# Optimization experiments

Measured on AMD Instinct MI355X. Metric: run time of the kernel, lower is better.

Reference implementation:

```python
import jax, jax.numpy as jnp
import numpy as np

B, S, D = 4, 4096, 1024
H = 8                    # num_heads
DK = D // H              # head_k_dim = 128
DV = D // H              # head_v_dim = 128
KLEPE = 5                # lepe kernel size
ROPE_BASE = 10000.0


def rotate_half(x):
    x1, x2 = jnp.split(x, 2, axis=-1)
    return jnp.concatenate([-x2, x1], axis=-1)


def rope_sin_cos(seq_len, dim):
    inv_freq = 1.0 / (ROPE_BASE ** (jnp.arange(0, dim, 2, dtype=jnp.float32) / dim))
    freqs = jnp.arange(seq_len, dtype=jnp.float32)[:, None] * inv_freq[None, :]
    emb = jnp.concatenate([freqs, freqs], axis=-1)  # [S, dim]
    return jnp.sin(emb), jnp.cos(emb)


def mala_attn(q, k, v):
    """Magnitude-aware linear attention with inline RoPE.

    Attention weights A_ij = (scale*q_i.k_j + 1) / (scale*q_i.(sum_j k_j) + S):
    rows sum to 1 but, unlike plain linear attention, the sharpness of the
    distribution still depends on ||q_i|| (magnitude rectification). Computed
    in O(S*d^2) linear form without materializing the SxS matrix.
    q, k: [B,S,H,DK]; v: [B,S,H,DV].
    """
    sin, cos = rope_sin_cos(q.shape[1], q.shape[-1])
    sin, cos = sin[None, :, None, :], cos[None, :, None, :]
    q = q * cos + rotate_half(q) * sin
    k = k * cos + rotate_half(k) * sin
    scale = q.shape[-1] ** -0.5
    seq_len = q.shape[1]
    kv = jnp.einsum('bshd,bshe->bhde', k, v)      # [B,H,DK,DV]
    ksum = k.sum(axis=1)                          # [B,H,DK]
    vsum = v.sum(axis=1)                          # [B,H,DV]
    num = jnp.einsum('bshd,bhde->bshe', q, kv) * scale + vsum[:, None, :, :]
    den = jnp.einsum('bshd,bhd->bsh', q, ksum) * scale + seq_len
    return num / den[..., None]


def lepe_conv(v, w, b):
    # depthwise Conv1d over the sequence axis; channel id = h*DV + d
    Bb, Ss = v.shape[0], v.shape[1]
    x = v.transpose(0, 2, 3, 1).reshape(Bb, H * DV, Ss)   # [B, C, S]
    y = jax.lax.conv_general_dilated(
        x, w, window_strides=(1,), padding=[(KLEPE // 2, KLEPE // 2)],
        dimension_numbers=('NCH', 'OIH', 'NCH'), feature_group_count=H * DV)
    y = y + b[None, :, None]
    return y.reshape(Bb, H, DV, Ss).transpose(0, 3, 1, 2)  # [B,S,H,DV]


def setup_inputs() -> dict:
    key = jax.random.key(0)
    ks = jax.random.split(key, 8)
    w = 0.02
    return {
        'hidden_states': jax.random.normal(ks[0], (B, S, D), dtype=jnp.float32),
        'Wq': jax.random.normal(ks[1], (D, D), dtype=jnp.float32) * w,
        'Wk': jax.random.normal(ks[2], (D, D), dtype=jnp.float32) * w,
        'Wv': jax.random.normal(ks[3], (D, D), dtype=jnp.float32) * w,
        'Wg': jax.random.normal(ks[4], (D, D), dtype=jnp.float32) * w,
        'Wo': jax.random.normal(ks[5], (D, D), dtype=jnp.float32) * w,
        'lepe_w': jax.random.normal(ks[6], (D, 1, KLEPE), dtype=jnp.float32) * 0.1,
        'lepe_b': jnp.zeros((D,), dtype=jnp.float32),
    }


def reference(hidden_states, Wq, Wk, Wv, Wg, Wo, lepe_w, lepe_b):
    Bb, Ss, _ = hidden_states.shape
    q = (hidden_states @ Wq.T).reshape(Bb, Ss, H, DK)
    k = (hidden_states @ Wk.T).reshape(Bb, Ss, H, DK)
    v = (hidden_states @ Wv.T).reshape(Bb, Ss, H, DV)
    o_gate = hidden_states @ Wg.T                          # [B,S,D]
    o = mala_attn(q, k, v) + lepe_conv(v, lepe_w, lepe_b)  # [B,S,H,DV]
    o = o.reshape(Bb, Ss, H * DV) * o_gate
    return o @ Wo.T
```

## Files before the change

kernel.cpp:

```cpp
#include <hip/hip_runtime.h>
#include <math.h>
#include <stdint.h>


typedef __bf16 bf16;
typedef __bf16 bf16x2 __attribute__((ext_vector_type(2)));
typedef __bf16 bf16x4 __attribute__((ext_vector_type(4)));
typedef __bf16 bf16x8 __attribute__((ext_vector_type(8)));
typedef float f32x4 __attribute__((ext_vector_type(4)));

static constexpr float kScale = 0.08838834764831845f;

__device__ __forceinline__ void async_copy16(const void* g, void* l) {
  __builtin_amdgcn_global_load_lds(
      (const __attribute__((address_space(1))) void*)(uintptr_t)g,
      (__attribute__((address_space(3))) void*)(uintptr_t)l, 16, 0, 0);
}

__global__ __launch_bounds__(256, 2) void gemm_qkvg(
    const bf16* __restrict__ A, const bf16* __restrict__ Bw,
    bf16* __restrict__ C, const float2* __restrict__ tab)
{
  __shared__ __align__(16) char smem[17408];
  bf16* As = (bf16*)smem;
  bf16* Bs = (bf16*)(smem + 8192);
  bf16* T  = (bf16*)smem;

  const int t = threadIdx.x;
  const int bid = blockIdx.x;
  const int xcd = bid & 7, n = bid >> 3;
  const int bx = xcd * 16 + (n & 15);
  const int by = n >> 4;
  const long m0 = (long)bx * 128;
  A  += m0 * 1024;
  Bw += (long)by * 131072;
  C  += m0 * 4096 + (long)by * 128;

  const int i0 = t, i1 = t + 256;
  const bf16* gA0 = A  + (long)(i0 >> 2) * 1024 + (i0 & 3) * 8;
  const bf16* gA1 = A  + (long)(i1 >> 2) * 1024 + (i1 & 3) * 8;
  const bf16* gB0 = Bw + (long)(i0 >> 2) * 1024 + (i0 & 3) * 8;
  const bf16* gB1 = Bw + (long)(i1 >> 2) * 1024 + (i1 & 3) * 8;
  bf16* lA0 = As + i0 * 8; bf16* lA1 = As + i1 * 8;
  bf16* lB0 = Bs + i0 * 8; bf16* lB1 = Bs + i1 * 8;

  const int lane = t & 63, wv = t >> 6;
  const int moff = (wv & 1) * 64, noff = (wv >> 1) * 64;
  const int fm = lane & 15, fq = lane >> 4;

  f32x4 acc[4][4] = {};

  for (int k0 = 0; k0 < 1024; k0 += 32) {
    async_copy16(gA0, lA0); async_copy16(gA1, lA1);
    async_copy16(gB0, lB0); async_copy16(gB1, lB1);
    gA0 += 32; gA1 += 32; gB0 += 32; gB1 += 32;
    __syncthreads();
    bf16x8 af[4], bfv[4];
#pragma unroll
    for (int i = 0; i < 4; ++i) {
      af[i]  = *(const bf16x8*)(As + (moff + i * 16 + fm) * 32 + fq * 8);
      bfv[i] = *(const bf16x8*)(Bs + (noff + i * 16 + fm) * 32 + fq * 8);
    }
#pragma unroll
    for (int i = 0; i < 4; ++i)
#pragma unroll
      for (int j = 0; j < 4; ++j)
        acc[i][j] = __builtin_amdgcn_mfma_f32_16x16x32_bf16(af[i], bfv[j], acc[i][j], 0, 0, 0);
    __syncthreads();
  }

#pragma unroll
  for (int half = 0; half < 2; ++half) {
    if ((wv & 1) == half) {
#pragma unroll
      for (int i = 0; i < 4; ++i)
#pragma unroll
        for (int j = 0; j < 4; ++j)
#pragma unroll
          for (int r = 0; r < 4; ++r)
            T[(i * 16 + fq * 4 + r) * 136 + noff + j * 16 + fm] = (bf16)acc[i][j][r];
    }
    __syncthreads();
    if (by < 16) {
#pragma unroll
      for (int it = 0; it < 16; ++it) {
        const int pi = t + it * 256;
        const int row = pi >> 6, i = pi & 63;
        const int s = (int)((m0 + half * 64 + row) & 4095);
        const float2 sc = tab[s * 64 + i];
        float x1 = (float)T[row * 136 + i];
        float x2 = (float)T[row * 136 + i + 64];
        T[row * 136 + i]      = (bf16)(x1 * sc.y - x2 * sc.x);
        T[row * 136 + i + 64] = (bf16)(x2 * sc.y + x1 * sc.x);
      }
      __syncthreads();
    }
    const int srow0 = t >> 4, sc0 = (t & 15) * 8;
#pragma unroll
    for (int it = 0; it < 4; ++it) {
      const int row = it * 16 + srow0;
      *(bf16x8*)(C + (long)(half * 64 + row) * 4096 + sc0) = *(const bf16x8*)(T + row * 136 + sc0);
    }
    __syncthreads();
  }
}

__global__ __launch_bounds__(256, 2) void gemm_final(
    const bf16* __restrict__ A, const bf16* __restrict__ Bw,
    float* __restrict__ C)
{
  __shared__ __align__(16) bf16 As[128 * 32];
  __shared__ __align__(16) bf16 Bs[128 * 32];
  const int t = threadIdx.x;
  const int bid = blockIdx.x;
  const int xcd = bid & 7, n = bid >> 3;
  const int bx = xcd * 16 + (n & 15);
  const int by = n >> 4;
  const long m0 = (long)bx * 128;
  A  += m0 * 1024;
  Bw += (long)by * 131072;
  C  += m0 * 1024 + (long)by * 128;

  const int i0 = t, i1 = t + 256;
  const bf16* gA0 = A  + (long)(i0 >> 2) * 1024 + (i0 & 3) * 8;
  const bf16* gA1 = A  + (long)(i1 >> 2) * 1024 + (i1 & 3) * 8;
  const bf16* gB0 = Bw + (long)(i0 >> 2) * 1024 + (i0 & 3) * 8;
  const bf16* gB1 = Bw + (long)(i1 >> 2) * 1024 + (i1 & 3) * 8;
  bf16* lA0 = As + i0 * 8; bf16* lA1 = As + i1 * 8;
  bf16* lB0 = Bs + i0 * 8; bf16* lB1 = Bs + i1 * 8;

  const int lane = t & 63, wv = t >> 6;
  const int moff = (wv & 1) * 64, noff = (wv >> 1) * 64;
  const int fm = lane & 15, fq = lane >> 4;

  f32x4 acc[4][4] = {};

  for (int k0 = 0; k0 < 1024; k0 += 32) {
    async_copy16(gA0, lA0); async_copy16(gA1, lA1);
    async_copy16(gB0, lB0); async_copy16(gB1, lB1);
    gA0 += 32; gA1 += 32; gB0 += 32; gB1 += 32;
    __syncthreads();
    bf16x8 af[4], bfv[4];
#pragma unroll
    for (int i = 0; i < 4; ++i) {
      af[i]  = *(const bf16x8*)(As + (moff + i * 16 + fm) * 32 + fq * 8);
      bfv[i] = *(const bf16x8*)(Bs + (noff + i * 16 + fm) * 32 + fq * 8);
    }
#pragma unroll
    for (int i = 0; i < 4; ++i)
#pragma unroll
      for (int j = 0; j < 4; ++j)
        acc[i][j] = __builtin_amdgcn_mfma_f32_16x16x32_bf16(af[i], bfv[j], acc[i][j], 0, 0, 0);
    __syncthreads();
  }

#pragma unroll
  for (int i = 0; i < 4; ++i)
#pragma unroll
    for (int j = 0; j < 4; ++j)
#pragma unroll
      for (int r = 0; r < 4; ++r)
        C[(long)(moff + i * 16 + fq * 4 + r) * 1024 + noff + j * 16 + fm] = acc[i][j][r];
}

__global__ __launch_bounds__(256, 2) void gemm_num(
    const bf16* __restrict__ QKVG, const bf16* __restrict__ kvTall,
    const float* __restrict__ ksum, const float* __restrict__ vsum,
    const float* __restrict__ lepe_w, const float* __restrict__ lepe_b,
    bf16* __restrict__ obuf)
{
  __shared__ __align__(16) char smem[17408];
  bf16* As = (bf16*)smem;
  bf16* Bs = (bf16*)(smem + 8192);
  bf16* T  = (bf16*)smem;
  __shared__ float sden[128], svsum[128], slb[128], sksum[128];
  __shared__ float slw[5][128];

  const int t = threadIdx.x;
  const int h = blockIdx.y, b = blockIdx.z;
  const int bh = b * 8 + h;
  const long m0 = (long)blockIdx.x * 128;
  const bf16* A  = QKVG + (long)b * 16777216 + m0 * 4096 + h * 128;
  const bf16* Bw = kvTall + (long)bh * 16384;

  if (t < 128) {
    sksum[t] = ksum[bh * 128 + t];
    svsum[t] = vsum[bh * 128 + t];
    slb[t]   = lepe_b[h * 128 + t];
#pragma unroll
    for (int j = 0; j < 5; ++j) slw[j][t] = lepe_w[(h * 128 + t) * 5 + j];
  }

  const int i0 = t, i1 = t + 256;
  const bf16* gA0 = A + (long)(i0 >> 2) * 4096 + (i0 & 3) * 8;
  const bf16* gA1 = A + (long)(i1 >> 2) * 4096 + (i1 & 3) * 8;
  const bf16* gB0 = Bw + (long)(i0 >> 2) * 128 + (i0 & 3) * 8;
  const bf16* gB1 = Bw + (long)(i1 >> 2) * 128 + (i1 & 3) * 8;
  bf16* lA0 = As + i0 * 8; bf16* lA1 = As + i1 * 8;
  bf16* lB0 = Bs + i0 * 8; bf16* lB1 = Bs + i1 * 8;

  const int lane = t & 63, wv = t >> 6;
  const int moff = (wv & 1) * 64, noff = (wv >> 1) * 64;
  const int fm = lane & 15, fq = lane >> 4;

  f32x4 acc[4][4] = {};
  float dacc = 0.f;

  for (int k0 = 0; k0 < 128; k0 += 32) {
    async_copy16(gA0, lA0); async_copy16(gA1, lA1);
    async_copy16(gB0, lB0); async_copy16(gB1, lB1);
    gA0 += 32; gA1 += 32; gB0 += 32; gB1 += 32;
    __syncthreads();
    bf16x8 af[4], bfv[4];
#pragma unroll
    for (int i = 0; i < 4; ++i) {
      af[i]  = *(const bf16x8*)(As + (moff + i * 16 + fm) * 32 + fq * 8);
      bfv[i] = *(const bf16x8*)(Bs + (noff + i * 16 + fm) * 32 + fq * 8);
    }
#pragma unroll
    for (int i = 0; i < 4; ++i)
#pragma unroll
      for (int j = 0; j < 4; ++j)
        acc[i][j] = __builtin_amdgcn_mfma_f32_16x16x32_bf16(af[i], bfv[j], acc[i][j], 0, 0, 0);
    if (t < 128) {
#pragma unroll
      for (int c8 = 0; c8 < 4; ++c8) {
        bf16x8 q8 = *(const bf16x8*)(As + t * 32 + c8 * 8);
#pragma unroll
        for (int e = 0; e < 8; ++e) dacc += (float)q8[e] * sksum[k0 + c8 * 8 + e];
      }
    }
    __syncthreads();
  }
  if (t < 128) sden[t] = dacc * kScale + 4096.0f;

  const int c2 = lane * 2;
  const float w0[5] = {slw[0][c2], slw[1][c2], slw[2][c2], slw[3][c2], slw[4][c2]};
  const float w1[5] = {slw[0][c2+1], slw[1][c2+1], slw[2][c2+1], slw[3][c2+1], slw[4][c2+1]};
  const float lb0 = slb[c2], lb1 = slb[c2 + 1];

#pragma unroll
  for (int half = 0; half < 2; ++half) {
    if ((wv & 1) == half) {
#pragma unroll
      for (int i = 0; i < 4; ++i)
#pragma unroll
        for (int j = 0; j < 4; ++j)
#pragma unroll
          for (int r = 0; r < 4; ++r) {
            const int col = noff + j * 16 + fm;
            T[(i * 16 + fq * 4 + r) * 136 + col] = (bf16)(acc[i][j][r] * kScale + svsum[col]);
          }
    }
    __syncthreads();
    for (int rr = 0; rr < 16; ++rr) {
      const int lrow = wv * 16 + rr;
      const int row = half * 64 + lrow;
      const int s = (int)(m0 + row);
      const long grow = (long)b * 4096 + s;
      const float rden = 1.0f / sden[row];
      const bf16* vrow = QKVG + grow * 4096 + 2048 + h * 128 + c2;
      bf16x2 a2 = *(const bf16x2*)(T + lrow * 136 + c2);
      float lep0 = lb0, lep1 = lb1;
#pragma unroll
      for (int jt = 0; jt < 5; ++jt) {
        const int srow = s + jt - 2;
        if (srow >= 0 && srow < 4096) {
          bf16x2 v2 = *(const bf16x2*)(vrow + (long)(jt - 2) * 4096);
          lep0 += (float)v2[0] * w0[jt];
          lep1 += (float)v2[1] * w1[jt];
        }
      }
      bf16x2 g2 = *(const bf16x2*)(QKVG + grow * 4096 + 3072 + h * 128 + c2);
      bf16x2 o2;
      o2[0] = (bf16)(((float)a2[0] * rden + lep0) * (float)g2[0]);
      o2[1] = (bf16)(((float)a2[1] * rden + lep1) * (float)g2[1]);
      *(bf16x2*)(obuf + grow * 1024 + h * 128 + c2) = o2;
    }
    __syncthreads();
  }
}

__global__ void prep_kernel(const float* __restrict__ X, const float* __restrict__ Wq,
                            const float* __restrict__ Wk, const float* __restrict__ Wv,
                            const float* __restrict__ Wg, const float* __restrict__ Wo,
                            bf16* __restrict__ Xb, bf16* __restrict__ Wcat,
                            bf16* __restrict__ Wob, float2* __restrict__ tab)
{
  const int blk = blockIdx.x;
  if (blk < 16384) {
    long g = ((long)blk * 256 + threadIdx.x) * 4;
    float4 v = *(const float4*)(X + g);
    bf16x4 o = {(bf16)v.x, (bf16)v.y, (bf16)v.z, (bf16)v.w};
    *(bf16x4*)(Xb + g) = o;
  } else if (blk < 21504) {
    long g = ((long)(blk - 16384) * 256 + threadIdx.x) * 4;
    if (g < 4194304) {
      long idx = g & 1048575;
      int sel = (int)(g >> 20);
      const float* s = sel == 0 ? Wq : sel == 1 ? Wk : sel == 2 ? Wv : Wg;
      float4 v = *(const float4*)(s + idx);
      bf16x4 o = {(bf16)v.x, (bf16)v.y, (bf16)v.z, (bf16)v.w};
      *(bf16x4*)(Wcat + g) = o;
    } else {
      long idx = g - 4194304;
      float4 v = *(const float4*)(Wo + idx);
      bf16x4 o = {(bf16)v.x, (bf16)v.y, (bf16)v.z, (bf16)v.w};
      *(bf16x4*)(Wob + idx) = o;
    }
  } else {
    int idx = (blk - 21504) * 256 + threadIdx.x;
    int s = idx >> 6, i = idx & 63;
    float inv = powf(10000.0f, -((float)(2 * i)) / 128.0f);
    float ang = (float)s * inv;
    float sn, cs;
    sincosf(ang, &sn, &cs);
    tab[idx] = make_float2(sn, cs);
  }
}

__global__ __launch_bounds__(256, 2) void kv_mfma(
    const bf16* __restrict__ QKVG, float* __restrict__ kvp,
    float* __restrict__ ksump, float* __restrict__ vsump)
{
  __shared__ __align__(16) bf16 VT[128 * 40];
  __shared__ __align__(16) bf16 KT[128 * 40];
  const int t = threadIdx.x;
  const int chunk = blockIdx.x, bh = blockIdx.y;
  const int b = bh >> 3, h = bh & 7;
  const long rowbase = ((long)b * 4096 + chunk * 256) * 4096 + h * 128;
  const bf16* Kg = QKVG + rowbase + 1024;
  const bf16* Vg = QKVG + rowbase + 2048;

  const int sp = t >> 4, fc = t & 15;
  const int lane = t & 63, wv = t >> 6;
  const int eoff = (wv & 1) * 64, doff = (wv >> 1) * 64;
  const int fm = lane & 15, fq = lane >> 4;
  const int srow = t & 127;
  const bool sumK = t >= 128;

  f32x4 acc[4][4] = {};
  float rsum = 0.f;

  for (int sb = 0; sb < 256; sb += 32) {
    const long go = (long)(sb + 2 * sp) * 4096 + fc * 8;
    bf16x8 v0 = *(const bf16x8*)(Vg + go);
    bf16x8 v1 = *(const bf16x8*)(Vg + go + 4096);
    bf16x8 k0 = *(const bf16x8*)(Kg + go);
    bf16x8 k1 = *(const bf16x8*)(Kg + go + 4096);
#pragma unroll
    for (int j = 0; j < 8; ++j) {
      const int f = fc * 8 + j;
      bf16x2 vp2 = {v0[j], v1[j]};
      bf16x2 kp2 = {k0[j], k1[j]};
      *(bf16x2*)(VT + f * 40 + 2 * sp) = vp2;
      *(bf16x2*)(KT + f * 40 + 2 * sp) = kp2;
    }
    __syncthreads();
    bf16x8 af[4], bfv[4];
#pragma unroll
    for (int i = 0; i < 4; ++i) {
      af[i]  = *(const bf16x8*)(VT + (eoff + i * 16 + fm) * 40 + fq * 8);
      bfv[i] = *(const bf16x8*)(KT + (doff + i * 16 + fm) * 40 + fq * 8);
    }
#pragma unroll
    for (int i = 0; i < 4; ++i)
#pragma unroll
      for (int j = 0; j < 4; ++j)
        acc[i][j] = __builtin_amdgcn_mfma_f32_16x16x32_bf16(af[i], bfv[j], acc[i][j], 0, 0, 0);
    const bf16* rp = (sumK ? KT : VT) + srow * 40;
#pragma unroll
    for (int i = 0; i < 4; ++i) {
      bf16x8 r8 = *(const bf16x8*)(rp + i * 8);
#pragma unroll
      for (int j = 0; j < 8; ++j) rsum += (float)r8[j];
    }
    __syncthreads();
  }

  float* plane = kvp + ((long)chunk * 32 + bh) * 16384;
#pragma unroll
  for (int i = 0; i < 4; ++i)
#pragma unroll
    for (int j = 0; j < 4; ++j)
#pragma unroll
      for (int r = 0; r < 4; ++r)
        plane[(long)(eoff + i * 16 + fq * 4 + r) * 128 + (doff + j * 16 + fm)] = acc[i][j][r];
  float* sdst = (sumK ? ksump : vsump) + ((long)chunk * 32 + bh) * 128 + srow;
  *sdst = rsum;
}

__global__ void kv_reduce(const float* __restrict__ kvp, const float* __restrict__ ksump,
                          const float* __restrict__ vsump, bf16* __restrict__ kvT,
                          float* __restrict__ ksum, float* __restrict__ vsum)
{
  long g = (long)blockIdx.x * 256 + threadIdx.x;
  long bh = g >> 14, idx = g & 16383;
  float s = 0.f;
#pragma unroll
  for (int c = 0; c < 16; ++c) s += kvp[((long)c * 32 + bh) * 16384 + idx];
  kvT[g] = (bf16)s;
  if (g < 8192) {
    int bh2 = (int)(g >> 8), rem = (int)(g & 255), f = rem & 127;
    const float* src = (rem >> 7) ? ksump : vsump;
    float* dst = (rem >> 7) ? ksum : vsum;
    float s2 = 0.f;
#pragma unroll
    for (int c = 0; c < 16; ++c) s2 += src[((long)c * 32 + bh2) * 128 + f];
    dst[bh2 * 128 + f] = s2;
  }
}

extern "C" void kernel_launch(void* const* d_in, const int* in_sizes, int n_in,
                              void* d_out, int out_size, void* d_ws, size_t ws_size,
                              hipStream_t stream)
{
  const float* X      = (const float*)d_in[0];
  const float* Wq     = (const float*)d_in[1];
  const float* Wk     = (const float*)d_in[2];
  const float* Wv     = (const float*)d_in[3];
  const float* Wg     = (const float*)d_in[4];
  const float* Wo     = (const float*)d_in[5];
  const float* lepe_w = (const float*)d_in[6];
  const float* lepe_b = (const float*)d_in[7];
  float* out = (float*)d_out;

  char* ws = (char*)d_ws;
  bf16*   Xb    = (bf16*)(ws);
  float*  kvp   = (float*)(ws);
  bf16*   Wcat  = (bf16*)(ws + 33554432);
  bf16*   Wob   = (bf16*)(ws + 41943040);
  float2* tab   = (float2*)(ws + 44040192);
  float*  ksump = (float*)(ws + 44040192);
  float*  vsump = (float*)(ws + 44302336);
  bf16*   QKVG  = (bf16*)(ws + 46137344);
  float*  ksum  = (float*)(ws + 180355072);
  float*  vsum  = (float*)(ws + 180371456);
  bf16*   kvT   = (bf16*)(ws + 180387840);
  bf16*   obuf  = (bf16*)(ws + 181960704);

  prep_kernel<<<22528, 256, 0, stream>>>(X, Wq, Wk, Wv, Wg, Wo, Xb, Wcat, Wob, tab);

  gemm_qkvg<<<4096, 256, 0, stream>>>(Xb, Wcat, QKVG, tab);

  kv_mfma<<<dim3(16, 32), 256, 0, stream>>>(QKVG, kvp, ksump, vsump);
  kv_reduce<<<2048, 256, 0, stream>>>(kvp, ksump, vsump, kvT, ksum, vsum);

  gemm_num<<<dim3(32, 8, 4), 256, 0, stream>>>(QKVG, kvT, ksum, vsum, lepe_w, lepe_b, obuf);

  gemm_final<<<1024, 256, 0, stream>>>(obuf, Wob, out);
}
```

Measured before the change: 448.8 us.

## Rewrite QKVG GEMM as 256x256 double-buffered pipelined kernel with swizzled LDS

Result: no change. 452.7 us (+0.9%).

```diff
diff --git a/kernel.cpp b/kernel.cpp
--- a/kernel.cpp
+++ b/kernel.cpp
@@ -17,89 +17,197 @@
       (__attribute__((address_space(3))) void*)(uintptr_t)l, 16, 0, 0);
 }
 
-__global__ __launch_bounds__(256, 2) void gemm_qkvg(
+__global__ __launch_bounds__(512, 1) void gemm_qkvg(
     const bf16* __restrict__ A, const bf16* __restrict__ Bw,
     bf16* __restrict__ C, const float2* __restrict__ tab)
 {
-  __shared__ __align__(16) char smem[17408];
-  bf16* As = (bf16*)smem;
-  bf16* Bs = (bf16*)(smem + 8192);
-  bf16* T  = (bf16*)smem;
+  __shared__ __align__(16) char smem[131072];
 
   const int t = threadIdx.x;
   const int bid = blockIdx.x;
-  const int xcd = bid & 7, n = bid >> 3;
-  const int bx = xcd * 16 + (n & 15);
-  const int by = n >> 4;
-  const long m0 = (long)bx * 128;
-  A  += m0 * 1024;
-  Bw += (long)by * 131072;
-  C  += m0 * 4096 + (long)by * 128;
-
-  const int i0 = t, i1 = t + 256;
-  const bf16* gA0 = A  + (long)(i0 >> 2) * 1024 + (i0 & 3) * 8;
-  const bf16* gA1 = A  + (long)(i1 >> 2) * 1024 + (i1 & 3) * 8;
-  const bf16* gB0 = Bw + (long)(i0 >> 2) * 1024 + (i0 & 3) * 8;
-  const bf16* gB1 = Bw + (long)(i1 >> 2) * 1024 + (i1 & 3) * 8;
-  bf16* lA0 = As + i0 * 8; bf16* lA1 = As + i1 * 8;
-  bf16* lB0 = Bs + i0 * 8; bf16* lB1 = Bs + i1 * 8;
-
-  const int lane = t & 63, wv = t >> 6;
-  const int moff = (wv & 1) * 64, noff = (wv >> 1) * 64;
+  const int swz = (bid & 7) * 128 + (bid >> 3);
+  const int bx = swz & 63;
+  const int by = swz >> 6;
+  const long m0 = (long)bx * 256;
+  const long n0 = (long)by * 256;
+
+  const int d0 = t * 16;
+  const int dd = d0 ^ (((d0 >> 9) & 1) << 5);
+  const int rT = dd >> 7;
+  const int cT = (dd & 127) >> 1;
+  const bf16* aSt = A  + (m0 + rT) * 1024 + cT;
+  const bf16* bSt = Bw + (n0 + rT) * 1024 + cT;
+  char* ldsDst = smem + d0;
+
+  const int lane = t & 63, wid = t >> 6;
+  const int wm = wid >> 2, wn = wid & 3;
   const int fm = lane & 15, fq = lane >> 4;
-
-  f32x4 acc[4][4] = {};
-
-  for (int k0 = 0; k0 < 1024; k0 += 32) {
-    async_copy16(gA0, lA0); async_copy16(gA1, lA1);
-    async_copy16(gB0, lB0); async_copy16(gB1, lB1);
-    gA0 += 32; gA1 += 32; gB0 += 32; gB1 += 32;
-    __syncthreads();
-    bf16x8 af[4], bfv[4];
-#pragma unroll
-    for (int i = 0; i < 4; ++i) {
-      af[i]  = *(const bf16x8*)(As + (moff + i * 16 + fm) * 32 + fq * 8);
-      bfv[i] = *(const bf16x8*)(Bs + (noff + i * 16 + fm) * 32 + fq * 8);
-    }
-#pragma unroll
-    for (int i = 0; i < 4; ++i)
-#pragma unroll
-      for (int j = 0; j < 4; ++j)
-        acc[i][j] = __builtin_amdgcn_mfma_f32_16x16x32_bf16(af[i], bfv[j], acc[i][j], 0, 0, 0);
-    __syncthreads();
-  }
-
-#pragma unroll
-  for (int half = 0; half < 2; ++half) {
-    if ((wv & 1) == half) {
-#pragma unroll
-      for (int i = 0; i < 4; ++i)
-#pragma unroll
-        for (int j = 0; j < 4; ++j)
+  const int xsw = (fm & 4) << 3;
+  const char* ldsA = smem + wm * 16384 + fm * 128 + (fq * 16 ^ xsw);
+  const char* ldsB = smem + 32768 + (wn >> 1) * 16384 +
+                     ((wn & 1) * 64 + fm) * 128 + (fq * 16 ^ xsw);
+
+  f32x4 acc[8][4] = {};
+  bf16x8 a4[4][2], b2[2][2];
+
+#define STAGE_A(kt, h) do {                                                  \
+    const bf16* s_ = aSt + (long)(h) * 131072 + (kt) * 64;                   \
+    char* d_ = ldsDst + ((kt) & 1) * 65536 + (h) * 16384;                    \
+    async_copy16(s_, d_);                                                    \
+    async_copy16(s_ + 65536, d_ + 8192);                                     \
+  } while (0)
+#define STAGE_B(kt, h) do {                                                  \
+    const bf16* s_ = bSt + (long)(h) * 131072 + (kt) * 64;                   \
+    char* d_ = ldsDst + ((kt) & 1) * 65536 + 32768 + (h) * 16384;            \
+    async_copy16(s_, d_);                                                    \
+    async_copy16(s_ + 65536, d_ + 8192);                                     \
+  } while (0)
+#define LOAD_A(buf, qi) do {                                                 \
+    const char* p_ = ldsA + (buf) * 65536 + (qi) * 8192;                     \
+    a4[0][0] = *(const bf16x8*)(p_);                                         \
+    a4[0][1] = *(const bf16x8*)(p_ + 64);                                    \
+    a4[1][0] = *(const bf16x8*)(p_ + 2048);                                  \
+    a4[1][1] = *(const bf16x8*)(p_ + 2048 + 64);                             \
+    a4[2][0] = *(const bf16x8*)(p_ + 4096);                                  \
+    a4[2][1] = *(const bf16x8*)(p_ + 4096 + 64);                             \
+    a4[3][0] = *(const bf16x8*)(p_ + 6144);                                  \
+    a4[3][1] = *(const bf16x8*)(p_ + 6144 + 64);                             \
+  } while (0)
+#define LOAD_B(buf, qj) do {                                                 \
+    const char* p_ = ldsB + (buf) * 65536 + (qj) * 4096;                     \
+    b2[0][0] = *(const bf16x8*)(p_);                                         \
+    b2[0][1] = *(const bf16x8*)(p_ + 64);                                    \
+    b2[1][0] = *(const bf16x8*)(p_ + 2048);                                  \
+    b2[1][1] = *(const bf16x8*)(p_ + 2048 + 64);                             \
+  } while (0)
+#define MM1(i, j, ks)                                                        \
+    acc[i][j] = __builtin_amdgcn_mfma_f32_16x16x32_bf16(                     \
+        a4[(i) & 3][ks], b2[(j) & 1][ks], acc[i][j], 0, 0, 0)
+#define MFMA_Q(qi, qj) do {                                                  \
+    MM1(4*(qi)+0, 2*(qj)+0, 0); MM1(4*(qi)+1, 2*(qj)+0, 0);                  \
+    MM1(4*(qi)+2, 2*(qj)+0, 0); MM1(4*(qi)+3, 2*(qj)+0, 0);                  \
+    MM1(4*(qi)+0, 2*(qj)+1, 0); MM1(4*(qi)+1, 2*(qj)+1, 0);                  \
+    MM1(4*(qi)+2, 2*(qj)+1, 0); MM1(4*(qi)+3, 2*(qj)+1, 0);                  \
+    MM1(4*(qi)+0, 2*(qj)+0, 1); MM1(4*(qi)+1, 2*(qj)+0, 1);                  \
+    MM1(4*(qi)+2, 2*(qj)+0, 1); MM1(4*(qi)+3, 2*(qj)+0, 1);                  \
+    MM1(4*(qi)+0, 2*(qj)+1, 1); MM1(4*(qi)+1, 2*(qj)+1, 1);                  \
+    MM1(4*(qi)+2, 2*(qj)+1, 1); MM1(4*(qi)+3, 2*(qj)+1, 1);                  \
+  } while (0)
+#define BAR()    __builtin_amdgcn_s_barrier()
+#define SCHEDB() __builtin_amdgcn_sched_barrier(0)
+#define PRIO(p)  __builtin_amdgcn_s_setprio(p)
+
+  STAGE_A(0, 0); STAGE_A(0, 1); STAGE_B(0, 0); STAGE_B(0, 1);
+  STAGE_A(1, 0);
+  asm volatile("s_waitcnt vmcnt(2)" ::: "memory");
+  BAR(); SCHEDB();
+
+#pragma unroll 1
+  for (int it = 0; it < 7; ++it) {
+    const int k1 = 2 * it + 1;
+    const int k2 = 2 * it + 2;
+    const int k3 = 2 * it + 3;
+    LOAD_A(0, 0); LOAD_B(0, 0);
+    STAGE_A(k1, 1);
+    BAR(); SCHEDB(); PRIO(1); MFMA_Q(0, 0); PRIO(0); BAR(); SCHEDB();
+    LOAD_B(0, 1);
+    STAGE_B(k1, 0);
+    BAR(); SCHEDB(); PRIO(1); MFMA_Q(0, 1); PRIO(0); BAR(); SCHEDB();
+    LOAD_A(0, 1);
+    STAGE_B(k1, 1);
+    BAR(); SCHEDB(); PRIO(1); MFMA_Q(1, 1); PRIO(0); BAR(); SCHEDB();
+    LOAD_B(0, 0);
+    STAGE_A(k2, 0);
+    BAR(); SCHEDB(); PRIO(1); MFMA_Q(1, 0); PRIO(0);
+    asm volatile("s_waitcnt vmcnt(2)" ::: "memory");
+    BAR(); SCHEDB();
+    LOAD_A(1, 0); LOAD_B(1, 0);
+    STAGE_A(k2, 1);
+    BAR(); SCHEDB(); PRIO(1); MFMA_Q(0, 0); PRIO(0); BAR(); SCHEDB();
+    LOAD_B(1, 1);
+    STAGE_B(k2, 0);
+    BAR(); SCHEDB(); PRIO(1); MFMA_Q(0, 1); PRIO(0); BAR(); SCHEDB();
+    LOAD_A(1, 1);
+    STAGE_B(k2, 1);
+    BAR(); SCHEDB(); PRIO(1); MFMA_Q(1, 1); PRIO(0); BAR(); SCHEDB();
+    LOAD_B(1, 0);
+    STAGE_A(k3, 0);
+    BAR(); SCHEDB(); PRIO(1); MFMA_Q(1, 0); PRIO(0);
+    asm volatile("s_waitcnt vmcnt(2)" ::: "memory");
+    BAR(); SCHEDB();
+  }
+
+  {
+    LOAD_A(0, 0); LOAD_B(0, 0);
+    STAGE_A(15, 1);
+    BAR(); SCHEDB(); PRIO(1); MFMA_Q(0, 0); PRIO(0); BAR(); SCHEDB();
+    LOAD_B(0, 1);
+    STAGE_B(15, 0);
+    BAR(); SCHEDB(); PRIO(1); MFMA_Q(0, 1); PRIO(0); BAR(); SCHEDB();
+    LOAD_A(0, 1);
+    STAGE_B(15, 1);
+    BAR(); SCHEDB(); PRIO(1); MFMA_Q(1, 1); PRIO(0); BAR(); SCHEDB();
+    LOAD_B(0, 0);
+    BAR(); SCHEDB(); PRIO(1); MFMA_Q(1, 0); PRIO(0);
+    asm volatile("s_waitcnt vmcnt(0)" ::: "memory");
+    BAR(); SCHEDB();
+    LOAD_A(1, 0); LOAD_B(1, 0);
+    BAR(); SCHEDB(); PRIO(1); MFMA_Q(0, 0); PRIO(0); BAR(); SCHEDB();
+    LOAD_B(1, 1);
+    BAR(); SCHEDB(); PRIO(1); MFMA_Q(0, 1); PRIO(0); BAR(); SCHEDB();
+    LOAD_A(1, 1);
+    BAR(); SCHEDB(); PRIO(1); MFMA_Q(1, 1); PRIO(0); BAR(); SCHEDB();
+    LOAD_B(1, 0);
+    BAR(); SCHEDB(); PRIO(1); MFMA_Q(1, 0); PRIO(0); BAR(); SCHEDB();
+  }
+
+#undef STAGE_A
+#undef STAGE_B
+#undef LOAD_A
+#undef LOAD_B
+#undef MM1
+#undef MFMA_Q
+#undef BAR
+#undef SCHEDB
+#undef PRIO
+
+  bf16* T = (bf16*)smem;
+  __syncthreads();
+#pragma unroll 1
+  for (int hw = 0; hw < 2; ++hw) {
+    if (wm == hw) {
+#pragma unroll
+      for (int rf = 0; rf < 8; ++rf)
+#pragma unroll
+        for (int cf = 0; cf < 4; ++cf)
 #pragma unroll
           for (int r = 0; r < 4; ++r)
-            T[(i * 16 + fq * 4 + r) * 136 + noff + j * 16 + fm] = (bf16)acc[i][j][r];
-    }
-    __syncthreads();
-    if (by < 16) {
-#pragma unroll
-      for (int it = 0; it < 16; ++it) {
-        const int pi = t + it * 256;
-        const int row = pi >> 6, i = pi & 63;
-        const int s = (int)((m0 + half * 64 + row) & 4095);
+            T[(rf * 16 + fq * 4 + r) * 264 + wn * 64 + cf * 16 + fm] =
+                (bf16)acc[rf][cf][r];
+    }
+    __syncthreads();
+    if (by < 8) {
+#pragma unroll
+      for (int ii = 0; ii < 32; ++ii) {
+        const int pi = t + ii * 512;
+        const int row = pi >> 7, pr = pi & 127;
+        const int hd = pr >> 6, i = pr & 63;
+        const int c0 = hd * 128 + i;
+        const int s = (int)((m0 + hw * 128 + row) & 4095);
         const float2 sc = tab[s * 64 + i];
-        float x1 = (float)T[row * 136 + i];
-        float x2 = (float)T[row * 136 + i + 64];
-        T[row * 136 + i]      = (bf16)(x1 * sc.y - x2 * sc.x);
-        T[row * 136 + i + 64] = (bf16)(x2 * sc.y + x1 * sc.x);
+        float x1 = (float)T[row * 264 + c0];
+        float x2 = (float)T[row * 264 + c0 + 64];
+        T[row * 264 + c0]      = (bf16)(x1 * sc.y - x2 * sc.x);
+        T[row * 264 + c0 + 64] = (bf16)(x2 * sc.y + x1 * sc.x);
       }
       __syncthreads();
     }
-    const int srow0 = t >> 4, sc0 = (t & 15) * 8;
-#pragma unroll
-    for (int it = 0; it < 4; ++it) {
-      const int row = it * 16 + srow0;
-      *(bf16x8*)(C + (long)(half * 64 + row) * 4096 + sc0) = *(const bf16x8*)(T + row * 136 + sc0);
+#pragma unroll
+    for (int ii = 0; ii < 8; ++ii) {
+      const int cid = t + ii * 512;
+      const int row = cid >> 5, ch = cid & 31;
+      *(bf16x8*)(C + (m0 + hw * 128 + row) * 4096 + n0 + ch * 8) =
+          *(const bf16x8*)(T + row * 264 + ch * 8);
     }
     __syncthreads();
   }
@@ -441,7 +549,7 @@
 
   prep_kernel<<<22528, 256, 0, stream>>>(X, Wq, Wk, Wv, Wg, Wo, Xb, Wcat, Wob, tab);
 
-  gemm_qkvg<<<4096, 256, 0, stream>>>(Xb, Wcat, QKVG, tab);
+  gemm_qkvg<<<1024, 512, 0, stream>>>(Xb, Wcat, QKVG, tab);
 
   kv_mfma<<<dim3(16, 32), 256, 0, stream>>>(QKVG, kvp, ksump, vsump);
   kv_reduce<<<2048, 256, 0, stream>>>(kvp, ksump, vsump, kvT, ksum, vsum);
```
